# Kernel optimization log

Measured on AMD Instinct MI355X. Metric: run time of the kernel, lower is better.

The kernel has to match this reference:

```python
import jax, jax.numpy as jnp
import numpy as np

NUM_EMBEDDINGS = 1024
EMBEDDING_DIM = 16
COMMITMENT_COST = 0.25
B, H, W = 16, 64, 64


def setup_inputs() -> dict:
    key = jax.random.key(0)
    k1, k2 = jax.random.split(key)
    z = jax.random.normal(k1, (B, H, W, EMBEDDING_DIM), dtype=jnp.float32)
    # nn.Embedding init: uniform(-1/num_embeddings, 1/num_embeddings)
    lim = 1.0 / NUM_EMBEDDINGS
    embedding_weight = jax.random.uniform(
        k2, (NUM_EMBEDDINGS, EMBEDDING_DIM), dtype=jnp.float32,
        minval=-lim, maxval=lim)
    return {"z": z, "embedding_weight": embedding_weight}


def reference(z, embedding_weight):
    b, h, w, c = z.shape
    flat_z = z.reshape(-1, c)  # [N, D]
    # squared L2 distances: ||z||^2 + ||e||^2 - 2 z.e
    distances = (
        jnp.sum(flat_z ** 2, axis=1, keepdims=True)
        + jnp.sum(embedding_weight ** 2, axis=1)
        - 2.0 * flat_z @ embedding_weight.T
    )  # [N, K]
    encoding_indices = jnp.argmin(distances, axis=1)  # [N]
    z_q = embedding_weight[encoding_indices].reshape(z.shape)
    loss = (
        jnp.mean((jax.lax.stop_gradient(z_q) - z) ** 2)
        + COMMITMENT_COST * jnp.mean((z_q - jax.lax.stop_gradient(z)) ** 2)
    )
    z_q_st = z + jax.lax.stop_gradient(z_q - z)  # straight-through
    return z_q_st, loss, encoding_indices.reshape(b, h, w)
```

## Files before the change

### kernel.cpp

```cpp
#include <hip/hip_runtime.h>
#include <string.h>


typedef __bf16 bf16x8 __attribute__((ext_vector_type(8)));
typedef float  f32x16 __attribute__((ext_vector_type(16)));

constexpr int BLOCK = 512;
constexpr int NROWS = 65536;
constexpr int K = 1024;
constexpr int RPB = 128;
constexpr int NBLK = NROWS / RPB;
constexpr int TPW = 16;
constexpr int CAP = 192;
constexpr float BAND = 1.5e-3f;
constexpr int OFF_LOSS = 1048576;
constexpr int OFF_IDX  = 1048577;

__device__ __forceinline__ float np_sumsq16(const float* a) {
  float s[16];
#pragma unroll
  for (int j = 0; j < 16; ++j) s[j] = __fmul_rn(a[j], a[j]);
  float r[8];
#pragma unroll
  for (int j = 0; j < 8; ++j) r[j] = __fadd_rn(s[j], s[j + 8]);
  const float t0 = __fadd_rn(r[0], r[1]);
  const float t1 = __fadd_rn(r[2], r[3]);
  const float t2 = __fadd_rn(r[4], r[5]);
  const float t3 = __fadd_rn(r[6], r[7]);
  return __fadd_rn(__fadd_rn(t0, t1), __fadd_rn(t2, t3));
}

__device__ __forceinline__ float np_dist(const float* zz, const float* ee,
                                         float z2, float e2k) {
  float c0 = zz[0]*ee[0];   c0 = fmaf(zz[1],ee[1],c0);   c0 = fmaf(zz[2],ee[2],c0);   c0 = fmaf(zz[3],ee[3],c0);
  float c1 = zz[4]*ee[4];   c1 = fmaf(zz[5],ee[5],c1);   c1 = fmaf(zz[6],ee[6],c1);   c1 = fmaf(zz[7],ee[7],c1);
  float c2 = zz[8]*ee[8];   c2 = fmaf(zz[9],ee[9],c2);   c2 = fmaf(zz[10],ee[10],c2); c2 = fmaf(zz[11],ee[11],c2);
  float c3 = zz[12]*ee[12]; c3 = fmaf(zz[13],ee[13],c3); c3 = fmaf(zz[14],ee[14],c3); c3 = fmaf(zz[15],ee[15],c3);
  const float dot = __fadd_rn(__fadd_rn(c0, c1), __fadd_rn(c2, c3));
  return __fmaf_rn(-2.0f, dot, __fadd_rn(z2, e2k));
}

__global__ __launch_bounds__(256)
void vq_pre(const float* __restrict__ emb, float* __restrict__ e2g,
            char* __restrict__ Bpack) {
  const int r = blockIdx.x * 256 + threadIdx.x;
  const float4* g4 = reinterpret_cast<const float4*>(emb);
  float ee[16];
  float4* ev = reinterpret_cast<float4*>(ee);
#pragma unroll
  for (int j = 0; j < 4; ++j) ev[j] = g4[r * 4 + j];
  e2g[r] = np_sumsq16(ee);
  unsigned int wd[8];
#pragma unroll
  for (int j = 0; j < 8; ++j) {
    __bf16 lo = (__bf16)ee[2*j], hi = (__bf16)ee[2*j+1];
    unsigned short ulo, uhi;
    memcpy(&ulo, &lo, 2); memcpy(&uhi, &hi, 2);
    wd[j] = (unsigned int)ulo | ((unsigned int)uhi << 16);
  }
  const int tt = r >> 5, c = r & 31;
  *reinterpret_cast<uint4*>(Bpack + tt*1024 + c*16)       = make_uint4(wd[0], wd[1], wd[2], wd[3]);
  *reinterpret_cast<uint4*>(Bpack + tt*1024 + 512 + c*16) = make_uint4(wd[4], wd[5], wd[6], wd[7]);
}

__global__ __launch_bounds__(BLOCK, 4)
void vq_main(const float* __restrict__ z, const float* __restrict__ emb,
             const float* __restrict__ e2g, const char* __restrict__ Bpack,
             float* __restrict__ out, float* __restrict__ partials) {
  __shared__ unsigned int sclist[8][CAP];
  __shared__ unsigned long long smin64[4][32];
  __shared__ float smin[8][32];
  __shared__ int   scnt[8];
  __shared__ float sred[8];

  const int t = threadIdx.x;
  const int lane = t & 63;
  const int w = t >> 6;
  const int pair = w >> 1;
  const int h = lane >> 5;
  const int rr = lane & 31;

  const float4* g4 = reinterpret_cast<const float4*>(emb);
  const float4* z4 = reinterpret_cast<const float4*>(z);

  if (lane == 0) scnt[w] = 0;
  if (t < 128) smin64[t >> 5][t & 31] = ~0ull;

  const int wrow0 = blockIdx.x * RPB + pair * 32;
  const float* zrow = z + (size_t)(wrow0 + rr) * 16 + h * 8;
  const float4 a0 = *reinterpret_cast<const float4*>(zrow);
  const float4 a1 = *reinterpret_cast<const float4*>(zrow + 4);
  bf16x8 af;
  af[0]=(__bf16)a0.x; af[1]=(__bf16)a0.y; af[2]=(__bf16)a0.z; af[3]=(__bf16)a0.w;
  af[4]=(__bf16)a1.x; af[5]=(__bf16)a1.y; af[6]=(__bf16)a1.z; af[7]=(__bf16)a1.w;

  const int kt0 = (w & 1) * TPW;
  const bf16x8* bfp = reinterpret_cast<const bf16x8*>(Bpack + (size_t)lane * 16);

  float e2r[TPW];
#pragma unroll
  for (int j = 0; j < TPW; ++j) e2r[j] = e2g[(kt0 + j) * 32 + rr] + 0.5f;

  float runm[16];
#pragma unroll
  for (int i = 0; i < 16; ++i) runm[i] = __builtin_inff();

#pragma unroll 4
  for (int tt = kt0; tt < kt0 + TPW; ++tt) {
    f32x16 zc = {};
    f32x16 acc = __builtin_amdgcn_mfma_f32_32x32x16_bf16(af, bfp[tt * 64], zc, 0, 0, 0);
    const float pre = e2r[tt - kt0];
#pragma unroll
    for (int i = 0; i < 16; ++i)
      runm[i] = fminf(runm[i], __fmaf_rn(-2.0f, acc[i], pre));
  }

#pragma unroll
  for (int i = 0; i < 16; ++i)
#pragma unroll
    for (int m = 1; m < 32; m <<= 1)
      runm[i] = fminf(runm[i], __shfl_xor(runm[i], m));

  if (rr == 0) {
#pragma unroll
    for (int i = 0; i < 16; ++i)
      smin[w][(i & 3) + 8 * (i >> 2) + 4 * h] = runm[i];
  }
  __syncthreads();
#pragma unroll
  for (int i = 0; i < 16; ++i)
    runm[i] = fminf(runm[i], smin[w ^ 1][(i & 3) + 8 * (i >> 2) + 4 * h]) + BAND;

#pragma unroll 4
  for (int tt = kt0; tt < kt0 + TPW; ++tt) {
    f32x16 zc = {};
    f32x16 acc = __builtin_amdgcn_mfma_f32_32x32x16_bf16(af, bfp[tt * 64], zc, 0, 0, 0);
    const float pre = e2r[tt - kt0];
    const int kcol = tt * 32 + rr;
#pragma unroll
    for (int i = 0; i < 16; ++i) {
      const float m = __fmaf_rn(-2.0f, acc[i], pre);
      if (m <= runm[i]) {
        const int rowloc = (i & 3) + 8 * (i >> 2) + 4 * h;
        const int slot = atomicAdd(&scnt[w], 1);
        if (slot < CAP) sclist[w][slot] = ((unsigned)rowloc << 16) | (unsigned)kcol;
      }
    }
  }
  int cnt = scnt[w]; if (cnt > CAP) cnt = CAP;

  for (int j0 = 0; j0 < cnt; j0 += 64) {
    const int j = j0 + lane;
    if (j < cnt) {
      const unsigned ent = sclist[w][j];
      const int rowj = (int)(ent >> 16), kj = (int)(ent & 1023);
      float zz[16]; float4* zv = reinterpret_cast<float4*>(zz);
#pragma unroll
      for (int q = 0; q < 4; ++q) zv[q] = z4[(size_t)(wrow0 + rowj) * 4 + q];
      float ee[16]; float4* ev = reinterpret_cast<float4*>(ee);
#pragma unroll
      for (int q = 0; q < 4; ++q) ev[q] = g4[(size_t)kj * 4 + q];
      const float d = np_dist(zz, ee, np_sumsq16(zz), e2g[kj]);
      const unsigned long long key =
          ((unsigned long long)__float_as_uint(d) << 32) | (unsigned long long)kj;
      atomicMin(&smin64[pair][rowj], key);
    }
  }
  __syncthreads();

  float lsum = 0.0f;
  if (!(w & 1) && lane < 32) {
    const int bk = (int)(smin64[pair][lane] & 1023ull);
    const int r = wrow0 + lane;
    float zz[16]; float4* zv = reinterpret_cast<float4*>(zz);
#pragma unroll
    for (int q = 0; q < 4; ++q) zv[q] = z4[(size_t)r * 4 + q];
    float ee[16]; float4* ev = reinterpret_cast<float4*>(ee);
#pragma unroll
    for (int q = 0; q < 4; ++q) ev[q] = g4[(size_t)bk * 4 + q];
    float ov[16];
#pragma unroll
    for (int j2 = 0; j2 < 16; ++j2) {
      const float d = __fsub_rn(ee[j2], zz[j2]);
      lsum = fmaf(d, d, lsum);
      ov[j2] = __fadd_rn(zz[j2], d);
    }
    float4* o4 = reinterpret_cast<float4*>(out) + (size_t)r * 4;
    const float4* ovv = reinterpret_cast<const float4*>(ov);
#pragma unroll
    for (int q = 0; q < 4; ++q) o4[q] = ovv[q];
    out[OFF_IDX + r] = (float)bk;
  }

#pragma unroll
  for (int off = 32; off > 0; off >>= 1) lsum += __shfl_down(lsum, off);
  if (lane == 0) sred[w] = lsum;
  __syncthreads();
  if (t == 0)
    partials[blockIdx.x] = ((sred[0] + sred[1]) + (sred[2] + sred[3]))
                         + ((sred[4] + sred[5]) + (sred[6] + sred[7]));
}

__global__ __launch_bounds__(256)
void vq_fin(const float* __restrict__ partials, float* __restrict__ out) {
  const int t = threadIdx.x;
  float v = partials[t] + partials[t + 256];
#pragma unroll
  for (int off = 32; off > 0; off >>= 1) v += __shfl_down(v, off);
  __shared__ float s[4];
  if ((t & 63) == 0) s[t >> 6] = v;
  __syncthreads();
  if (t == 0) {
    const float S = (s[0] + s[1]) + (s[2] + s[3]);
    const float m = S / 1048576.0f;
    out[OFF_LOSS] = 1.25f * m;
  }
}

extern "C" void kernel_launch(void* const* d_in, const int* in_sizes, int n_in,
                              void* d_out, int out_size, void* d_ws, size_t ws_size,
                              hipStream_t stream) {
  const float* z   = reinterpret_cast<const float*>(d_in[0]);
  const float* emb = reinterpret_cast<const float*>(d_in[1]);
  float* out       = reinterpret_cast<float*>(d_out);
  float* e2g       = reinterpret_cast<float*>(d_ws);
  float* partials  = e2g + K;
  char*  Bpack     = reinterpret_cast<char*>(e2g + 2048);
  vq_pre <<<K / 256, 256, 0, stream>>>(emb, e2g, Bpack);
  vq_main<<<NBLK, BLOCK, 0, stream>>>(z, emb, e2g, Bpack, out, partials);
  vq_fin <<<1, 256, 0, stream>>>(partials, out);
}
```

Before: 36.57 us.

## Fuse codebook preprocessing into main kernel, dropping vq_pre launch

Removes the separate vq_pre kernel. Each main block now computes all 1024 codebook squared norms into shared memory, and the MFMA B fragments are built on the fly by loading fp32 codebook rows and converting them to bf16 inside both distance passes. This saves one kernel launch and the global round trip through the workspace. In exchange it adds redundant per-block norm computation (each block reads the whole 64KB codebook), an extra __syncthreads, and twice as many B loads plus conversion work in the hot MFMA loops.

```diff
diff --git a/kernel.cpp b/kernel.cpp
--- a/kernel.cpp
+++ b/kernel.cpp
@@ -40,33 +40,19 @@
   return __fmaf_rn(-2.0f, dot, __fadd_rn(z2, e2k));
 }
 
-__global__ __launch_bounds__(256)
-void vq_pre(const float* __restrict__ emb, float* __restrict__ e2g,
-            char* __restrict__ Bpack) {
-  const int r = blockIdx.x * 256 + threadIdx.x;
-  const float4* g4 = reinterpret_cast<const float4*>(emb);
-  float ee[16];
-  float4* ev = reinterpret_cast<float4*>(ee);
-#pragma unroll
-  for (int j = 0; j < 4; ++j) ev[j] = g4[r * 4 + j];
-  e2g[r] = np_sumsq16(ee);
-  unsigned int wd[8];
-#pragma unroll
-  for (int j = 0; j < 8; ++j) {
-    __bf16 lo = (__bf16)ee[2*j], hi = (__bf16)ee[2*j+1];
-    unsigned short ulo, uhi;
-    memcpy(&ulo, &lo, 2); memcpy(&uhi, &hi, 2);
-    wd[j] = (unsigned int)ulo | ((unsigned int)uhi << 16);
-  }
-  const int tt = r >> 5, c = r & 31;
-  *reinterpret_cast<uint4*>(Bpack + tt*1024 + c*16)       = make_uint4(wd[0], wd[1], wd[2], wd[3]);
-  *reinterpret_cast<uint4*>(Bpack + tt*1024 + 512 + c*16) = make_uint4(wd[4], wd[5], wd[6], wd[7]);
+__device__ __forceinline__ bf16x8 load_bfrag(const float4* g4, int tt, int rr, int h) {
+  const float4 b0 = g4[(tt * 32 + rr) * 4 + 2 * h];
+  const float4 b1 = g4[(tt * 32 + rr) * 4 + 2 * h + 1];
+  bf16x8 bf;
+  bf[0]=(__bf16)b0.x; bf[1]=(__bf16)b0.y; bf[2]=(__bf16)b0.z; bf[3]=(__bf16)b0.w;
+  bf[4]=(__bf16)b1.x; bf[5]=(__bf16)b1.y; bf[6]=(__bf16)b1.z; bf[7]=(__bf16)b1.w;
+  return bf;
 }
 
 __global__ __launch_bounds__(BLOCK, 4)
 void vq_main(const float* __restrict__ z, const float* __restrict__ emb,
-             const float* __restrict__ e2g, const char* __restrict__ Bpack,
              float* __restrict__ out, float* __restrict__ partials) {
+  __shared__ float se2[K];
   __shared__ unsigned int sclist[8][CAP];
   __shared__ unsigned long long smin64[4][32];
   __shared__ float smin[8][32];
@@ -85,6 +71,16 @@
 
   if (lane == 0) scnt[w] = 0;
   if (t < 128) smin64[t >> 5][t & 31] = ~0ull;
+
+#pragma unroll
+  for (int n = 0; n < 2; ++n) {
+    const int c = t + n * BLOCK;
+    float ee[16];
+    float4* ev = reinterpret_cast<float4*>(ee);
+#pragma unroll
+    for (int j = 0; j < 4; ++j) ev[j] = g4[c * 4 + j];
+    se2[c] = np_sumsq16(ee);
+  }
 
   const int wrow0 = blockIdx.x * RPB + pair * 32;
   const float* zrow = z + (size_t)(wrow0 + rr) * 16 + h * 8;
@@ -95,11 +91,12 @@
   af[4]=(__bf16)a1.x; af[5]=(__bf16)a1.y; af[6]=(__bf16)a1.z; af[7]=(__bf16)a1.w;
 
   const int kt0 = (w & 1) * TPW;
-  const bf16x8* bfp = reinterpret_cast<const bf16x8*>(Bpack + (size_t)lane * 16);
+
+  __syncthreads();
 
   float e2r[TPW];
 #pragma unroll
-  for (int j = 0; j < TPW; ++j) e2r[j] = e2g[(kt0 + j) * 32 + rr] + 0.5f;
+  for (int j = 0; j < TPW; ++j) e2r[j] = se2[(kt0 + j) * 32 + rr] + 0.5f;
 
   float runm[16];
 #pragma unroll
@@ -108,7 +105,7 @@
 #pragma unroll 4
   for (int tt = kt0; tt < kt0 + TPW; ++tt) {
     f32x16 zc = {};
-    f32x16 acc = __builtin_amdgcn_mfma_f32_32x32x16_bf16(af, bfp[tt * 64], zc, 0, 0, 0);
+    f32x16 acc = __builtin_amdgcn_mfma_f32_32x32x16_bf16(af, load_bfrag(g4, tt, rr, h), zc, 0, 0, 0);
     const float pre = e2r[tt - kt0];
 #pragma unroll
     for (int i = 0; i < 16; ++i)
@@ -134,7 +131,7 @@
 #pragma unroll 4
   for (int tt = kt0; tt < kt0 + TPW; ++tt) {
     f32x16 zc = {};
-    f32x16 acc = __builtin_amdgcn_mfma_f32_32x32x16_bf16(af, bfp[tt * 64], zc, 0, 0, 0);
+    f32x16 acc = __builtin_amdgcn_mfma_f32_32x32x16_bf16(af, load_bfrag(g4, tt, rr, h), zc, 0, 0, 0);
     const float pre = e2r[tt - kt0];
     const int kcol = tt * 32 + rr;
 #pragma unroll
@@ -160,7 +157,7 @@
       float ee[16]; float4* ev = reinterpret_cast<float4*>(ee);
 #pragma unroll
       for (int q = 0; q < 4; ++q) ev[q] = g4[(size_t)kj * 4 + q];
-      const float d = np_dist(zz, ee, np_sumsq16(zz), e2g[kj]);
+      const float d = np_dist(zz, ee, np_sumsq16(zz), se2[kj]);
       const unsigned long long key =
           ((unsigned long long)__float_as_uint(d) << 32) | (unsigned long long)kj;
       atomicMin(&smin64[pair][rowj], key);
@@ -223,10 +220,7 @@
   const float* z   = reinterpret_cast<const float*>(d_in[0]);
   const float* emb = reinterpret_cast<const float*>(d_in[1]);
   float* out       = reinterpret_cast<float*>(d_out);
-  float* e2g       = reinterpret_cast<float*>(d_ws);
-  float* partials  = e2g + K;
-  char*  Bpack     = reinterpret_cast<char*>(e2g + 2048);
-  vq_pre <<<K / 256, 256, 0, stream>>>(emb, e2g, Bpack);
-  vq_main<<<NBLK, BLOCK, 0, stream>>>(z, emb, e2g, Bpack, out, partials);
+  float* partials  = reinterpret_cast<float*>(d_ws);
+  vq_main<<<NBLK, BLOCK, 0, stream>>>(z, emb, out, partials);
   vq_fin <<<1, 256, 0, stream>>>(partials, out);
 }
```

After: 37.37 us. 1.02x slower.
